# Kernel optimization log

Hardware: AMD Instinct MI355X
Metric: run time of the kernel (lower is better)

## Reference

```python
import jax, jax.numpy as jnp
import numpy as np

DIM = 256
CTX_DIM = 768
GROUPS = 8
EPS = 1e-5


def setup_inputs() -> dict:
    key = jax.random.key(0)
    ks = jax.random.split(key, 16)
    B, C, H, W, L = 16, DIM, 64, 64, 77
    s_conv = 1.0 / np.sqrt(C * 9)
    s_q = 1.0 / np.sqrt(C)
    s_kv = 1.0 / np.sqrt(CTX_DIM)
    return {
        "x": jax.random.normal(ks[0], (B, C, H, W), jnp.float32),
        "context": jax.random.normal(ks[1], (B, L, CTX_DIM), jnp.float32),
        "conv_w": jax.random.uniform(ks[2], (C, C, 3, 3), jnp.float32, -s_conv, s_conv),
        "conv_b": jax.random.uniform(ks[3], (C,), jnp.float32, -s_conv, s_conv),
        "gn_w": jnp.ones((C,), jnp.float32),
        "gn_b": jnp.zeros((C,), jnp.float32),
        "wq": jax.random.uniform(ks[4], (C, C), jnp.float32, -s_q, s_q),
        "bq": jax.random.uniform(ks[5], (C,), jnp.float32, -s_q, s_q),
        "wk": jax.random.uniform(ks[6], (C, CTX_DIM), jnp.float32, -s_kv, s_kv),
        "bk": jax.random.uniform(ks[7], (C,), jnp.float32, -s_kv, s_kv),
        "wv": jax.random.uniform(ks[8], (C, CTX_DIM), jnp.float32, -s_kv, s_kv),
        "bv": jax.random.uniform(ks[9], (C,), jnp.float32, -s_kv, s_kv),
        "wo": jax.random.uniform(ks[10], (C, C), jnp.float32, -s_q, s_q),
        "bo": jax.random.uniform(ks[11], (C,), jnp.float32, -s_q, s_q),
    }


def _group_norm(h, gn_w, gn_b):
    B, C, H, W = h.shape
    g = h.reshape(B, GROUPS, C // GROUPS, H, W)
    mean = g.mean(axis=(2, 3, 4), keepdims=True)
    var = g.var(axis=(2, 3, 4), keepdims=True)
    g = (g - mean) * jax.lax.rsqrt(var + EPS)
    h = g.reshape(B, C, H, W)
    return h * gn_w[None, :, None, None] + gn_b[None, :, None, None]


def reference(x, context, conv_w, conv_b, gn_w, gn_b, wq, bq, wk, bk, wv, bv, wo, bo):
    B, C, H, W = x.shape
    # conv 3x3, padding=1 (NCHW, OIHW)
    h = jax.lax.conv_general_dilated(
        x, conv_w, window_strides=(1, 1), padding=((1, 1), (1, 1)),
        dimension_numbers=("NCHW", "OIHW", "NCHW"))
    h = h + conv_b[None, :, None, None]
    h = jax.nn.silu(_group_norm(h, gn_w, gn_b))
    # flatten spatial -> tokens: [B, HW, C]
    hf = h.reshape(B, C, H * W).transpose(0, 2, 1)
    q = hf @ wq.T + bq                     # [B, HW, C]
    k = context @ wk.T + bk                # [B, L, C]
    v = context @ wv.T + bv                # [B, L, C]
    scale = 1.0 / jnp.sqrt(jnp.asarray(C, q.dtype))
    att = jax.nn.softmax(jnp.einsum("bqc,bkc->bqk", q, k) * scale, axis=-1)
    o = jnp.einsum("bqk,bkc->bqc", att, v) @ wo.T + bo
    h_att = o.transpose(0, 2, 1).reshape(B, C, H, W)
    return x + h_att
```

## Files before the change

### kernel.cpp

```cpp
#include <hip/hip_runtime.h>
#include <stdint.h>

#define B_  16
#define C_  256
#define HW_ 4096
#define Hp  66
#define PP  4356
#define EPS_ 1e-5f

typedef unsigned short u16;
typedef unsigned int   u32;
typedef __attribute__((ext_vector_type(4))) float  f32x4;
typedef __attribute__((ext_vector_type(8))) __bf16 bf16x8;
typedef __attribute__((ext_vector_type(8))) u16    u16x8;

__device__ __forceinline__ float bf2f(u16 u){ u32 x = ((u32)u)<<16; float f; __builtin_memcpy(&f,&x,4); return f; }
__device__ __forceinline__ u16 f2bf(float f){ u32 x; __builtin_memcpy(&x,&f,4); u32 r = x + 0x7fffu + ((x>>16)&1u); return (u16)(r>>16); }

__device__ __forceinline__ void g2l16(const void* g, void* l){
  __builtin_amdgcn_global_load_lds((__attribute__((address_space(1))) void*)(void*)g,
                                   (__attribute__((address_space(3))) void*)l, 16, 0, 0);
}
__device__ __forceinline__ bf16x8 ldfrag(const u16* p){
  u16x8 r = *(const u16x8*)p;
  return __builtin_bit_cast(bf16x8, r);
}

__global__ __launch_bounds__(256) void k_prep(const float* __restrict__ x, u16* __restrict__ xpT,
    const float* __restrict__ conv_w, const float* __restrict__ wq, const float* __restrict__ wo,
    const float* __restrict__ wk, const float* __restrict__ wv, const float* __restrict__ ctx,
    u16* __restrict__ wBt, u16* __restrict__ wqB, u16* __restrict__ woB,
    u16* __restrict__ wkvB, u16* __restrict__ ctxB, float* __restrict__ stats){
  __shared__ float Lt[64*65];
  int bid = blockIdx.x; int tid = threadIdx.x;
  if(bid >= 1056){
    int i = (bid-1056)*256 + tid;
    if(i < 589824){
      int j = i&7, co = (i>>3)&255, atom = (i>>11)&3, g = i>>13;
      int t = g%9, cic = g/9;
      int ciF = cic*32 + atom*8 + j;
      wBt[i] = f2bf(conv_w[(co*256+ciF)*9 + t]); return;
    }
    i -= 589824;
    if(i < 65536){ wqB[i] = f2bf(wq[i]); return; } i -= 65536;
    if(i < 65536){ woB[i] = f2bf(wo[i]); return; } i -= 65536;
    if(i < 196608){ wkvB[i] = f2bf(wk[i]); return; } i -= 196608;
    if(i < 196608){ wkvB[196608+i] = f2bf(wv[i]); return; } i -= 196608;
    if(i < 946176){ ctxB[i] = f2bf(ctx[i]); return; } i -= 946176;
    if(i < 512){ stats[i] = 0.f; }
    return;
  }
  int b = bid/66, hh = bid - b*66;
  if(hh==0 || hh==65){
    for(int i=tid;i<32*264;i+=256){
      int pl = i/264, off = i - pl*264;
      u32* p = (u32*)(xpT + ((size_t)(b*32+pl)*PP + (size_t)hh*Hp)*8);
      p[off] = 0u;
    }
    return;
  }
  {
    int pl = tid>>3, q = tid&7;
    size_t base = ((size_t)(b*32+pl)*PP + (size_t)hh*Hp + (q>=4?65:0))*8;
    ((u32*)(xpT + base))[q&3] = 0u;
  }
  int h = hh-1;
  for(int cc=0; cc<4; cc++){
    int c0=cc*64;
    int ci = tid>>2, w0 = (tid&3)*16;
    const float* xs = x + ((size_t)(b*C_ + c0+ci)*HW_) + h*64 + w0;
    for(int j=0;j<4;j++){
      float4 v = *(const float4*)(xs + j*4);
      Lt[ci*65 + w0 + j*4 + 0] = v.x;
      Lt[ci*65 + w0 + j*4 + 1] = v.y;
      Lt[ci*65 + w0 + j*4 + 2] = v.z;
      Lt[ci*65 + w0 + j*4 + 3] = v.w;
    }
    __syncthreads();
    int w = tid>>2, cj = (tid&3)*16;
    union { u16 u[16]; uint4 v[2]; } outu;
    for(int j=0;j<16;j++) outu.u[j] = f2bf(Lt[(cj+j)*65 + w]);
    int chan = c0 + cj;
    int cic = chan>>5, at0 = (chan>>3)&3;
    u16* dst = xpT + (((size_t)(b*8+cic)*4 + at0)*PP + (size_t)hh*Hp + w + 1)*8;
    *(uint4*)dst = outu.v[0];
    *(uint4*)(dst + (size_t)PP*8) = outu.v[1];
    __syncthreads();
  }
}

__global__ __launch_bounds__(256, 2) void k_conv(const u16* __restrict__ xpT, const u16* __restrict__ wBt,
    const float* __restrict__ conv_b, u16* __restrict__ h, float* __restrict__ stats){
  __shared__ u16 As[2][264*32];
  __shared__ u16 Bs[2][256*32];
  int bid = blockIdx.x;
  int b = bid >> 5, hp = bid & 31;
  int tid = threadIdx.x;
  int w = tid>>6, lane = tid&63, ln = lane&15, qd = lane>>4;
  int wm = w&1, wn = w>>1;
  f32x4 acc[4][8] = {};
  int hr_[4], wp_[4];
  #pragma unroll
  for(int mf=0;mf<4;mf++){ int p = wm*64 + mf*16 + ln; hr_[mf] = p>>6; wp_[mf] = p&63; }

  #pragma unroll
  for(int r=0;r<5;r++){
    int c = r*256 + tid;
    if(c < 1056){
      int atom = c/264, ipix = c - atom*264;
      g2l16(xpT + (((size_t)(b*8+0)*4 + atom)*PP + hp*132 + ipix)*8, &As[0][c*8]);
    }
  }
  #pragma unroll
  for(int r=0;r<4;r++){
    int c = r*256 + tid;
    g2l16(wBt + (size_t)c*8, &Bs[0][c*8]);
  }
  __syncthreads();

  int cb = 0;
  for(int ci=0; ci<8; ci++){
    int ca = ci&1;
    for(int t=0;t<9;t++){
      int tn = t+1, cin = ci;
      if(tn==9){ tn=0; cin=ci+1; }
      if(cin < 8){
        #pragma unroll
        for(int r=0;r<4;r++){
          int c = r*256 + tid;
          g2l16(wBt + ((size_t)(cin*9+tn)*1024 + c)*8, &Bs[cb^1][c*8]);
        }
      }
      if(t<5 && ci<7){
        int c = t*256 + tid;
        if(c < 1056){
          int atom = c/264, ipix = c - atom*264;
          g2l16(xpT + (((size_t)(b*8+ci+1)*4 + atom)*PP + hp*132 + ipix)*8, &As[ca^1][c*8]);
        }
      }
      int dy = (t*11)>>5, dx = t - dy*3;
      bf16x8 af[4], bfv[8];
      #pragma unroll
      for(int mf=0;mf<4;mf++){
        int ipix = (hr_[mf]+dy)*66 + wp_[mf] + dx;
        af[mf] = ldfrag(&As[ca][(qd*264 + ipix)*8]);
      }
      #pragma unroll
      for(int nf=0;nf<8;nf++) bfv[nf] = ldfrag(&Bs[cb][(qd*256 + wn*128+nf*16+ln)*8]);
      #pragma unroll
      for(int mf=0;mf<4;mf++)
        #pragma unroll
        for(int nf=0;nf<8;nf++)
          acc[mf][nf] = __builtin_amdgcn_mfma_f32_16x16x32_bf16(af[mf], bfv[nf], acc[mf][nf], 0,0,0);
      __syncthreads();
      cb ^= 1;
    }
  }
  float s[4]={0,0,0,0}, q[4]={0,0,0,0};
  int p0 = hp*128;
  for(int nf=0;nf<8;nf++){
    int n = wn*128 + nf*16 + ln;
    float bias = conv_b[n];
    for(int mf=0;mf<4;mf++){
      for(int r=0;r<4;r++){
        int p = wm*64 + mf*16 + qd*4 + r;
        float v = acc[mf][nf][r] + bias;
        h[((size_t)(b*HW_ + p0 + p))*C_ + n] = f2bf(v);
        s[nf>>1]+=v; q[nf>>1]+=v*v;
      }
    }
  }
  for(int off=32;off>=1;off>>=1){
    #pragma unroll
    for(int g=0;g<4;g++){ s[g]+=__shfl_down(s[g],off,64); q[g]+=__shfl_down(q[g],off,64); }
  }
  if(lane==0){
    #pragma unroll
    for(int g=0;g<4;g++){
      atomicAdd(&stats[(b*8 + wn*4 + g)*2+0], s[g]);
      atomicAdd(&stats[(b*8 + wn*4 + g)*2+1], q[g]);
    }
  }
}

__global__ __launch_bounds__(256, 2) void k_qgn(const u16* __restrict__ hbuf, const u16* __restrict__ wqB,
    const float* __restrict__ stats, const float* __restrict__ gnw, const float* __restrict__ gnb,
    const float* __restrict__ bq, u16* __restrict__ qb){
  __shared__ u16 As[128*32];
  __shared__ u16 Bs[256*32];
  int mt = blockIdx.x;
  int b = mt >> 5;
  int tid = threadIdx.x;
  int w = tid>>6, lane = tid&63, ln = lane&15, qd = lane>>4;
  int wm = w&1, wn = w>>1;
  int pr = tid>>1, half = tid&1;
  const u16* hsrc = hbuf + ((size_t)(mt*128+pr))*256 + half*16;
  f32x4 acc[4][8] = {};
  uint4 ra0, ra1, rb0, rb1;
  ra0 = *(const uint4*)(hsrc);
  ra1 = *(const uint4*)(hsrc + 8);
  for(int kt=0; kt<8; kt++){
    float sm = stats[(b*8+kt)*2], qm = stats[(b*8+kt)*2+1];
    float mean = sm*(1.f/131072.f);
    float rstd = rsqrtf(qm*(1.f/131072.f) - mean*mean + EPS_);
    int c0 = kt*32 + half*16;
    float4 gw0 = *(const float4*)(gnw+c0), gw1 = *(const float4*)(gnw+c0+4);
    float4 gw2 = *(const float4*)(gnw+c0+8), gw3 = *(const float4*)(gnw+c0+12);
    float4 gb0 = *(const float4*)(gnb+c0), gb1 = *(const float4*)(gnb+c0+4);
    float4 gb2 = *(const float4*)(gnb+c0+8), gb3 = *(const float4*)(gnb+c0+12);
    float gwv[16] = {gw0.x,gw0.y,gw0.z,gw0.w, gw1.x,gw1.y,gw1.z,gw1.w,
                     gw2.x,gw2.y,gw2.z,gw2.w, gw3.x,gw3.y,gw3.z,gw3.w};
    float gbv[16] = {gb0.x,gb0.y,gb0.z,gb0.w, gb1.x,gb1.y,gb1.z,gb1.w,
                     gb2.x,gb2.y,gb2.z,gb2.w, gb3.x,gb3.y,gb3.z,gb3.w};
    u16 inu[16];
    ((uint4*)inu)[0] = ra0; ((uint4*)inu)[1] = ra1;
    u16 outu[16];
    #pragma unroll
    for(int j=0;j<16;j++){
      float v = bf2f(inu[j]);
      v = (v-mean)*rstd*gwv[j] + gbv[j];
      float s = v/(1.f+__expf(-v));
      outu[j] = f2bf(s);
    }
    u16* adst = &As[pr*32 + half*16];
    ((uint4*)adst)[0] = ((uint4*)outu)[0];
    ((uint4*)adst)[1] = ((uint4*)outu)[1];
    #pragma unroll
    for(int r=0;r<4;r++){
      int c = r*256 + tid;
      int co = c>>2, atom = c&3;
      g2l16(wqB + (size_t)co*256 + kt*32 + atom*8, &Bs[c*8]);
    }
    if(kt<7){
      rb0 = *(const uint4*)(hsrc + (kt+1)*32);
      rb1 = *(const uint4*)(hsrc + (kt+1)*32 + 8);
    }
    __syncthreads();
    bf16x8 af[4], bfv[8];
    #pragma unroll
    for(int mf=0;mf<4;mf++) af[mf] = ldfrag(&As[(wm*64+mf*16+ln)*32 + qd*8]);
    #pragma unroll
    for(int nf=0;nf<8;nf++) bfv[nf] = ldfrag(&Bs[(wn*128+nf*16+ln)*32 + qd*8]);
    #pragma unroll
    for(int mf=0;mf<4;mf++)
      #pragma unroll
      for(int nf=0;nf<8;nf++)
        acc[mf][nf] = __builtin_amdgcn_mfma_f32_16x16x32_bf16(af[mf], bfv[nf], acc[mf][nf], 0,0,0);
    __syncthreads();
    ra0 = rb0; ra1 = rb1;
  }
  for(int nf=0;nf<8;nf++){
    int n = wn*128 + nf*16 + ln;
    float bias = bq[n];
    for(int mf=0;mf<4;mf++){
      for(int r=0;r<4;r++){
        int ml = wm*64 + mf*16 + qd*4 + r;
        qb[((size_t)(mt*128+ml))*256 + n] = f2bf(acc[mf][nf][r]+bias);
      }
    }
  }
}

__global__ __launch_bounds__(256) void k_kvproj(const u16* __restrict__ ctxB, const u16* __restrict__ wkvB,
    const float* __restrict__ bk, const float* __restrict__ bv,
    u16* __restrict__ kb, u16* __restrict__ vT){
  __shared__ u16 As[64*128];
  __shared__ u16 Bs[64*128];
  int bid = blockIdx.x;
  int nt = bid & 7, mt = bid >> 3;
  int n0 = nt*64, m0 = mt*64;
  int tid=threadIdx.x, w=tid>>6, lane=tid&63, ln=lane&15, qd=lane>>4;
  int wm = w&1, wn = w>>1;
  f32x4 acc[2][2]={};
  for(int kt=0;kt<6;kt++){
    #pragma unroll
    for(int r=0;r<4;r++){
      int c = r*256 + tid;
      int row = c>>4, atom = c&15;
      g2l16(ctxB + ((size_t)(m0+row)*768 + kt*128 + atom*8), &As[c*8]);
      g2l16(wkvB + ((size_t)(n0+row)*768 + kt*128 + atom*8), &Bs[c*8]);
    }
    __syncthreads();
    #pragma unroll
    for(int kk=0;kk<4;kk++){
      bf16x8 af[2], bfv[2];
      #pragma unroll
      for(int mf=0;mf<2;mf++) af[mf]=ldfrag(&As[(wm*32+mf*16+ln)*128 + kk*32 + qd*8]);
      #pragma unroll
      for(int nf=0;nf<2;nf++) bfv[nf]=ldfrag(&Bs[(wn*32+nf*16+ln)*128 + kk*32 + qd*8]);
      #pragma unroll
      for(int mf=0;mf<2;mf++)
        #pragma unroll
        for(int nf=0;nf<2;nf++)
          acc[mf][nf]=__builtin_amdgcn_mfma_f32_16x16x32_bf16(af[mf],bfv[nf],acc[mf][nf],0,0,0);
    }
    __syncthreads();
  }
  for(int mf=0;mf<2;mf++) for(int nf=0;nf<2;nf++){
    int ng = n0 + wn*32 + nf*16 + ln;
    float bias = ng<256 ? bk[ng] : bv[ng-256];
    for(int r=0;r<4;r++){
      int mg = m0 + wm*32 + mf*16 + qd*4 + r;
      if(mg<1232){
        float v=acc[mf][nf][r]+bias;
        int bb=mg/77, l=mg-bb*77;
        if(ng<256) kb[((size_t)(bb*77+l))*256+ng]=f2bf(v);
        else vT[((size_t)(bb*256+(ng-256)))*96 + l]=f2bf(v);
      }
    }
  }
}

__global__ __launch_bounds__(256) void k_attn(const u16* __restrict__ qg, const u16* __restrict__ kb,
    const u16* __restrict__ vT, u16* __restrict__ ob){
  __shared__ u16 Qs[4096];
  __shared__ u16 KVs[4096];
  __shared__ u16 Sb[128*88];
  __shared__ u16 Pb[128*104];
  __shared__ float invr[128];
  int bid=blockIdx.x; int b=bid>>5, qt=bid&31; int p0=qt*128;
  int tid=threadIdx.x, w=tid>>6, lane=tid&63, ln=lane&15, qd=lane>>4;
  int srow=tid>>2, koff=(tid&3)*8;
  f32x4 Sa[2][5]={};
  for(int kt=0;kt<8;kt++){
    for(int j=0;j<2;j++){
      int m=srow+j*64;
      g2l16(qg + ((size_t)(b*HW_+p0+m)*256 + kt*32+koff), &Qs[(size_t)tid*8+j*2048]);
    }
    for(int j=0;j<2;j++){
      int cja = tid + j*256;
      if(cja < 320){
        int l = cja>>2, ko2=(cja&3)*8;
        g2l16(kb + ((size_t)(b*77+l)*256 + kt*32+ko2), &KVs[(size_t)cja*8]);
      }
    }
    __syncthreads();
    bf16x8 af[2], bfv[5];
    for(int mf=0;mf<2;mf++) af[mf]=ldfrag(&Qs[(w*32+mf*16+ln)*32+qd*8]);
    for(int nf=0;nf<5;nf++) bfv[nf]=ldfrag(&KVs[(nf*16+ln)*32+qd*8]);
    for(int mf=0;mf<2;mf++) for(int nf=0;nf<5;nf++)
      Sa[mf][nf]=__builtin_amdgcn_mfma_f32_16x16x32_bf16(af[mf],bfv[nf],Sa[mf][nf],0,0,0);
    __syncthreads();
  }
  for(int mf=0;mf<2;mf++) for(int nf=0;nf<5;nf++) for(int r=0;r<4;r++){
    int ml=w*32+mf*16+qd*4+r, nl=nf*16+ln;
    Sb[ml*88+nl]=f2bf(Sa[mf][nf][r]*0.0625f);
  }
  __syncthreads();
  if(tid<128){
    u16* srp = &Sb[tid*88];
    srp[77]=0xFF80u; srp[78]=0xFF80u; srp[79]=0xFF80u;
    float mx=-1e30f;
    #pragma unroll
    for(int c8=0;c8<10;c8++){
      u16x8 v = *(const u16x8*)(srp + c8*8);
      #pragma unroll
      for(int j=0;j<8;j++) mx = fmaxf(mx, bf2f(v[j]));
    }
    u16* prow = &Pb[tid*104];
    float sum=0.f;
    #pragma unroll
    for(int c8=0;c8<10;c8++){
      u16x8 v = *(const u16x8*)(srp + c8*8);
      u16x8 o;
      #pragma unroll
      for(int j=0;j<8;j++){ float e=__expf(bf2f(v[j])-mx); sum+=e; o[j]=f2bf(e); }
      *(u16x8*)(prow + c8*8) = o;
    }
    #pragma unroll
    for(int j=80;j<96;j++) prow[j]=0;
    invr[tid] = 1.f/sum;
  }
  __syncthreads();
  for(int nh=0;nh<2;nh++){
    f32x4 Oa[2][8]={};
    for(int kt2=0;kt2<3;kt2++){
      for(int j=0;j<2;j++){
        int chunk=tid+j*256;
        int co=chunk>>2, ko2=(chunk&3)*8;
        g2l16(vT + ((size_t)(b*256+nh*128+co)*96 + kt2*32+ko2), &KVs[(size_t)chunk*8]);
      }
      __syncthreads();
      bf16x8 af[2], bfv[8];
      for(int mf=0;mf<2;mf++) af[mf]=ldfrag(&Pb[(w*32+mf*16+ln)*104 + kt2*32+qd*8]);
      for(int nf=0;nf<8;nf++) bfv[nf]=ldfrag(&KVs[(nf*16+ln)*32+qd*8]);
      for(int mf=0;mf<2;mf++) for(int nf=0;nf<8;nf++)
        Oa[mf][nf]=__builtin_amdgcn_mfma_f32_16x16x32_bf16(af[mf],bfv[nf],Oa[mf][nf],0,0,0);
      __syncthreads();
    }
    for(int mf=0;mf<2;mf++){
      #pragma unroll
      for(int r=0;r<4;r++){
        int ml=w*32+mf*16+qd*4+r;
        float inv = invr[ml];
        for(int nf=0;nf<8;nf++){
          int nl=nh*128+nf*16+ln;
          ob[((size_t)(b*HW_+p0+ml))*256+nl]=f2bf(Oa[mf][nf][r]*inv);
        }
      }
    }
  }
}

__global__ __launch_bounds__(256) void k_oproj(const u16* __restrict__ ob, const u16* __restrict__ woB,
    const float* __restrict__ bo, const float* __restrict__ x, float* __restrict__ outp){
  __shared__ u16 As[128*32];
  __shared__ u16 Bs[128*32];
  int bid=blockIdx.x;
  int b=bid>>6; int rr=bid&63; int cm=rr>>5, pt=rr&31;
  int c0=cm*128, p0=pt*128;
  int tid=threadIdx.x, w=tid>>6, lane=tid&63, ln=lane&15, qd=lane>>4, wm=w>>1, wn=w&1;
  int srow=tid>>2, koff=(tid&3)*8;
  f32x4 acc[4][4]={};
  for(int kt=0;kt<8;kt++){
    for(int j=0;j<2;j++){
      int m=srow+j*64;
      g2l16(woB + ((size_t)(c0+m)*256 + kt*32+koff),        &As[(size_t)tid*8+j*2048]);
      g2l16(ob  + ((size_t)(b*HW_+p0+m)*256 + kt*32+koff),  &Bs[(size_t)tid*8+j*2048]);
    }
    __syncthreads();
    bf16x8 af[4], bfv[4];
    for(int mf=0;mf<4;mf++) af[mf]=ldfrag(&As[(wm*64+mf*16+ln)*32+qd*8]);
    for(int nf=0;nf<4;nf++) bfv[nf]=ldfrag(&Bs[(wn*64+nf*16+ln)*32+qd*8]);
    for(int mf=0;mf<4;mf++) for(int nf=0;nf<4;nf++)
      acc[mf][nf]=__builtin_amdgcn_mfma_f32_16x16x32_bf16(af[mf],bfv[nf],acc[mf][nf],0,0,0);
    __syncthreads();
  }
  for(int mf=0;mf<4;mf++) for(int r=0;r<4;r++){
    int cl=c0+wm*64+mf*16+qd*4+r;
    float bias=bo[cl];
    for(int nf=0;nf<4;nf++){
      int pl=p0+wn*64+nf*16+ln;
      size_t idx=((size_t)(b*C_+cl))*HW_+pl;
      outp[idx]=x[idx]+acc[mf][nf][r]+bias;
    }
  }
}

extern "C" void kernel_launch(void* const* d_in, const int* in_sizes, int n_in,
                              void* d_out, int out_size, void* d_ws, size_t ws_size,
                              hipStream_t stream){
  const float* x      = (const float*)d_in[0];
  const float* ctx    = (const float*)d_in[1];
  const float* conv_w = (const float*)d_in[2];
  const float* conv_b = (const float*)d_in[3];
  const float* gnw    = (const float*)d_in[4];
  const float* gnb    = (const float*)d_in[5];
  const float* wq     = (const float*)d_in[6];
  const float* bq     = (const float*)d_in[7];
  const float* wk     = (const float*)d_in[8];
  const float* bk     = (const float*)d_in[9];
  const float* wv     = (const float*)d_in[10];
  const float* bv     = (const float*)d_in[11];
  const float* wo     = (const float*)d_in[12];
  const float* bo     = (const float*)d_in[13];
  char* ws = (char*)d_ws;
  u16* xpT  = (u16*)(ws + 0);
  u16* wBt  = (u16*)(ws + 35684352);
  u16* wqB  = (u16*)(ws + 36864000);
  u16* wkvB = (u16*)(ws + 36995072);
  u16* woB  = (u16*)(ws + 37781504);
  u16* ctxB = (u16*)(ws + 37912576);
  u16* hbuf = (u16*)(ws + 39804928);
  u16* kbv  = (u16*)(ws + 73359360);
  u16* vT   = (u16*)(ws + 73990144);
  u16* obuf = (u16*)(ws + 74776576);
  float* stats = (float*)(ws + 108331008);
  u16* qb = xpT;
  float* outp = (float*)d_out;

  k_prep  <<<9106, 256, 0, stream>>>(x, xpT, conv_w, wq, wo, wk, wv, ctx, wBt, wqB, woB, wkvB, ctxB, stats);
  k_conv  <<<512,  256, 0, stream>>>(xpT, wBt, conv_b, hbuf, stats);
  k_qgn   <<<512,  256, 0, stream>>>(hbuf, wqB, stats, gnw, gnb, bq, qb);
  k_kvproj<<<160,  256, 0, stream>>>(ctxB, wkvB, bk, bv, kbv, vT);
  k_attn  <<<512,  256, 0, stream>>>(qb, kbv, vT, obuf);
  k_oproj <<<1024, 256, 0, stream>>>(obuf, woB, bo, x, outp);
}
```

Baseline: 389.5 us.

## Restructure conv A-tile loads and relax barrier waits with partial vmcnt

The conv kernel now loads only the 64 interior pixels of each padded row into LDS and writes the left and right padding columns as zeros once, instead of copying the full padded row. The A-tile prefetch is spread over four steps with one 16-byte load per thread. The full __syncthreads is replaced by an explicit s_waitcnt vmcnt(1)/vmcnt(0) plus a raw s_barrier, so the A prefetch still in flight can overlap the next step. The barrier after the final iteration is skipped. The aim is to cut wasted global-to-LDS traffic and barrier stalls, but it relies on hand-written waitcnt ordering, which could race if the in-flight load accounting is wrong.

```diff
diff --git a/kernel.cpp b/kernel.cpp
--- a/kernel.cpp
+++ b/kernel.cpp
@@ -102,60 +102,64 @@
   int hr_[4], wp_[4];
   #pragma unroll
   for(int mf=0;mf<4;mf++){ int p = wm*64 + mf*16 + ln; hr_[mf] = p>>6; wp_[mf] = p&63; }
+  int arow = tid>>6, apx = tid&63;
+
+  if(tid < 64){
+    int buf = tid>>5, k = tid&31;
+    int atom = k>>3, row = (k>>1)&3, side = k&1;
+    uint4 z = {0,0,0,0};
+    *(uint4*)&As[buf][(atom*264 + row*66 + side*65)*8] = z;
+  }
 
   #pragma unroll
-  for(int r=0;r<5;r++){
-    int c = r*256 + tid;
-    if(c < 1056){
-      int atom = c/264, ipix = c - atom*264;
-      g2l16(xpT + (((size_t)(b*8+0)*4 + atom)*PP + hp*132 + ipix)*8, &As[0][c*8]);
-    }
-  }
+  for(int r=0;r<4;r++)
+    g2l16(wBt + ((size_t)0*1024 + r*256 + tid)*8, &Bs[0][(r*256+tid)*8]);
   #pragma unroll
-  for(int r=0;r<4;r++){
-    int c = r*256 + tid;
-    g2l16(wBt + (size_t)c*8, &Bs[0][c*8]);
-  }
+  for(int r=0;r<4;r++)
+    g2l16(xpT + (((size_t)(b*8+0)*4 + r)*PP + hp*132 + arow*66 + 1 + apx)*8,
+          &As[0][(r*264 + arow*66 + 1 + apx)*8]);
   __syncthreads();
 
-  int cb = 0;
   for(int ci=0; ci<8; ci++){
-    int ca = ci&1;
+    int ab = ci&1;
+    int cin = ci<7 ? ci+1 : 7;
     for(int t=0;t<9;t++){
-      int tn = t+1, cin = ci;
-      if(tn==9){ tn=0; cin=ci+1; }
-      if(cin < 8){
+      int pb = (ci + t)&1;
+      int last = (ci==7) & (t==8);
+      if(!last){
+        int tn = t+1, cb2 = ci; if(tn==9){tn=0; cb2=ci+1;}
+        int g = cb2*9 + tn;
         #pragma unroll
-        for(int r=0;r<4;r++){
-          int c = r*256 + tid;
-          g2l16(wBt + ((size_t)(cin*9+tn)*1024 + c)*8, &Bs[cb^1][c*8]);
-        }
-      }
-      if(t<5 && ci<7){
-        int c = t*256 + tid;
-        if(c < 1056){
-          int atom = c/264, ipix = c - atom*264;
-          g2l16(xpT + (((size_t)(b*8+ci+1)*4 + atom)*PP + hp*132 + ipix)*8, &As[ca^1][c*8]);
-        }
-      }
+        for(int r=0;r<4;r++)
+          g2l16(wBt + ((size_t)g*1024 + r*256 + tid)*8, &Bs[pb^1][(r*256+tid)*8]);
+      }
+      if(t<4)
+        g2l16(xpT + (((size_t)(b*8+cin)*4 + t)*PP + hp*132 + arow*66 + 1 + apx)*8,
+              &As[ab^1][(t*264 + arow*66 + 1 + apx)*8]);
+
       int dy = (t*11)>>5, dx = t - dy*3;
       bf16x8 af[4], bfv[8];
       #pragma unroll
       for(int mf=0;mf<4;mf++){
         int ipix = (hr_[mf]+dy)*66 + wp_[mf] + dx;
-        af[mf] = ldfrag(&As[ca][(qd*264 + ipix)*8]);
-      }
-      #pragma unroll
-      for(int nf=0;nf<8;nf++) bfv[nf] = ldfrag(&Bs[cb][(qd*256 + wn*128+nf*16+ln)*8]);
+        af[mf] = ldfrag(&As[ab][(qd*264 + ipix)*8]);
+      }
+      #pragma unroll
+      for(int nf=0;nf<8;nf++) bfv[nf] = ldfrag(&Bs[pb][(qd*256 + wn*128+nf*16+ln)*8]);
       #pragma unroll
       for(int mf=0;mf<4;mf++)
         #pragma unroll
         for(int nf=0;nf<8;nf++)
           acc[mf][nf] = __builtin_amdgcn_mfma_f32_16x16x32_bf16(af[mf], bfv[nf], acc[mf][nf], 0,0,0);
-      __syncthreads();
-      cb ^= 1;
-    }
-  }
+
+      if(!last){
+        if(t<4) asm volatile("s_waitcnt vmcnt(1)" ::: "memory");
+        else    asm volatile("s_waitcnt vmcnt(0)" ::: "memory");
+        __builtin_amdgcn_s_barrier();
+      }
+    }
+  }
+
   float s[4]={0,0,0,0}, q[4]={0,0,0,0};
   int p0 = hp*128;
   for(int nf=0;nf<8;nf++){
```

After: 425.0 us. 1.09x slower.

## Enlarge conv tile to 256 pixels and stream weights into registers

Applied to the files above, without the earlier changes.

The conv kernel now uses 512-thread blocks, each covering 256 output pixels (four image rows) instead of 128, which halves the block count and doubles reuse of each weight tile. Weight fragments are no longer staged through LDS. Each wave reads them directly from global memory into registers with one-step prefetching, and the per-tap __syncthreads is dropped so only one barrier per input-channel chunk remains. The cost is higher register pressure from the extra bN fragments, and weight loads that come from global/L2 latency rather than LDS. There are also fewer blocks (256) to spread across the CUs.

```diff
diff --git a/kernel.cpp b/kernel.cpp
--- a/kernel.cpp
+++ b/kernel.cpp
@@ -89,75 +89,71 @@
   }
 }
 
-__global__ __launch_bounds__(256, 2) void k_conv(const u16* __restrict__ xpT, const u16* __restrict__ wBt,
+__global__ __launch_bounds__(512, 2) void k_conv(const u16* __restrict__ xpT, const u16* __restrict__ wBt,
     const float* __restrict__ conv_b, u16* __restrict__ h, float* __restrict__ stats){
-  __shared__ u16 As[2][264*32];
-  __shared__ u16 Bs[2][256*32];
+  __shared__ u16 As[2][4*396*8];
   int bid = blockIdx.x;
-  int b = bid >> 5, hp = bid & 31;
+  int b = bid >> 4, hp = bid & 15;
   int tid = threadIdx.x;
   int w = tid>>6, lane = tid&63, ln = lane&15, qd = lane>>4;
-  int wm = w&1, wn = w>>1;
+  int wm = w&3, wn = w>>2;
   f32x4 acc[4][8] = {};
   int hr_[4], wp_[4];
   #pragma unroll
   for(int mf=0;mf<4;mf++){ int p = wm*64 + mf*16 + ln; hr_[mf] = p>>6; wp_[mf] = p&63; }
-
-  #pragma unroll
-  for(int r=0;r<5;r++){
-    int c = r*256 + tid;
-    if(c < 1056){
-      int atom = c/264, ipix = c - atom*264;
-      g2l16(xpT + (((size_t)(b*8+0)*4 + atom)*PP + hp*132 + ipix)*8, &As[0][c*8]);
-    }
-  }
+  const u16* bbase = wBt + (size_t)qd*2048 + wn*1024 + ln*8;
+
   #pragma unroll
   for(int r=0;r<4;r++){
-    int c = r*256 + tid;
-    g2l16(wBt + (size_t)c*8, &Bs[0][c*8]);
-  }
+    int c = r*512 + tid;
+    if(c < 1584){
+      int atom = c/396, ipix = c - atom*396;
+      g2l16(xpT + (((size_t)(b*8+0)*4 + atom)*PP + hp*264 + ipix)*8, &As[0][c*8]);
+    }
+  }
+  bf16x8 bC[8], bN[8];
+  #pragma unroll
+  for(int nf=0;nf<8;nf++) bC[nf] = ldfrag(bbase + nf*128);
   __syncthreads();
 
-  int cb = 0;
   for(int ci=0; ci<8; ci++){
-    int ca = ci&1;
+    int ab = ci&1;
+    #pragma unroll
     for(int t=0;t<9;t++){
-      int tn = t+1, cin = ci;
-      if(tn==9){ tn=0; cin=ci+1; }
-      if(cin < 8){
+      int g = ci*9 + t;
+      if(g < 71){
         #pragma unroll
-        for(int r=0;r<4;r++){
-          int c = r*256 + tid;
-          g2l16(wBt + ((size_t)(cin*9+tn)*1024 + c)*8, &Bs[cb^1][c*8]);
+        for(int nf=0;nf<8;nf++) bN[nf] = ldfrag(bbase + (size_t)(g+1)*8192 + nf*128);
+      }
+      if(ci < 7 && t < 4){
+        int c = t*512 + tid;
+        if(c < 1584){
+          int atom = c/396, ipix = c - atom*396;
+          g2l16(xpT + (((size_t)(b*8+ci+1)*4 + atom)*PP + hp*264 + ipix)*8, &As[ab^1][c*8]);
         }
       }
-      if(t<5 && ci<7){
-        int c = t*256 + tid;
-        if(c < 1056){
-          int atom = c/264, ipix = c - atom*264;
-          g2l16(xpT + (((size_t)(b*8+ci+1)*4 + atom)*PP + hp*132 + ipix)*8, &As[ca^1][c*8]);
-        }
-      }
       int dy = (t*11)>>5, dx = t - dy*3;
-      bf16x8 af[4], bfv[8];
+      bf16x8 af[4];
       #pragma unroll
       for(int mf=0;mf<4;mf++){
         int ipix = (hr_[mf]+dy)*66 + wp_[mf] + dx;
-        af[mf] = ldfrag(&As[ca][(qd*264 + ipix)*8]);
-      }
-      #pragma unroll
-      for(int nf=0;nf<8;nf++) bfv[nf] = ldfrag(&Bs[cb][(qd*256 + wn*128+nf*16+ln)*8]);
+        af[mf] = ldfrag(&As[ab][((size_t)qd*396 + ipix)*8]);
+      }
       #pragma unroll
       for(int mf=0;mf<4;mf++)
         #pragma unroll
         for(int nf=0;nf<8;nf++)
-          acc[mf][nf] = __builtin_amdgcn_mfma_f32_16x16x32_bf16(af[mf], bfv[nf], acc[mf][nf], 0,0,0);
-      __syncthreads();
-      cb ^= 1;
-    }
-  }
+          acc[mf][nf] = __builtin_amdgcn_mfma_f32_16x16x32_bf16(af[mf], bC[nf], acc[mf][nf], 0,0,0);
+      if(g < 71){
+        #pragma unroll
+        for(int nf=0;nf<8;nf++) bC[nf] = bN[nf];
+      }
+    }
+    __syncthreads();
+  }
+
   float s[4]={0,0,0,0}, q[4]={0,0,0,0};
-  int p0 = hp*128;
+  int p0 = hp*256;
   for(int nf=0;nf<8;nf++){
     int n = wn*128 + nf*16 + ln;
     float bias = conv_b[n];
@@ -177,8 +173,9 @@
   if(lane==0){
     #pragma unroll
     for(int g=0;g<4;g++){
-      atomicAdd(&stats[(b*8 + wn*4 + g)*2+0], s[g]);
-      atomicAdd(&stats[(b*8 + wn*4 + g)*2+1], q[g]);
+      int gg = wn*4 + g;
+      atomicAdd(&stats[(b*8 + gg)*2+0], s[g]);
+      atomicAdd(&stats[(b*8 + gg)*2+1], q[g]);
     }
   }
 }
@@ -470,7 +467,7 @@
   float* outp = (float*)d_out;
 
   k_prep  <<<9106, 256, 0, stream>>>(x, xpT, conv_w, wq, wo, wk, wv, ctx, wBt, wqB, woB, wkvB, ctxB, stats);
-  k_conv  <<<512,  256, 0, stream>>>(xpT, wBt, conv_b, hbuf, stats);
+  k_conv  <<<256,  512, 0, stream>>>(xpT, wBt, conv_b, hbuf, stats);
   k_qgn   <<<512,  256, 0, stream>>>(hbuf, wqB, stats, gnw, gnb, bq, qb);
   k_kvproj<<<160,  256, 0, stream>>>(ctxB, wkvB, bk, bv, kbv, vT);
   k_attn  <<<512,  256, 0, stream>>>(qb, kbv, vT, obuf);
```

Result: slower. 397.5 us (+2.1%).
